# Kernel tuning notes

Hardware: AMD Instinct MI355X
Metric: run time of the kernel (lower is better)

The kernel has to match this reference:

```python
import jax, jax.numpy as jnp
import numpy as np

N_BINS = 15  # matches ECELoss(n_bins=15)


def setup_inputs() -> dict:
    key = jax.random.key(0)
    k1, k2 = jax.random.split(key)
    B, C = 2_097_152, 16
    logits = jax.random.normal(k1, (B, C), dtype=jnp.float32) * 2.0
    # binary multi-label targets, stored as float (forward casts to float anyway)
    targets = (jax.random.uniform(k2, (B, C)) < 0.5).astype(jnp.float32)
    return {"logits": logits, "targets": targets}


def reference(logits, targets):
    """Vectorized ECE: single bucketize + segment-sum pass replacing the
    per-class/per-bin Python loops. Same math: for each non-empty (class, bin)
    cell, accumulate |mean_conf - mean_acc| * (cell_count / B), then divide by
    the number of non-empty cells."""
    B, C = logits.shape
    probs = jax.nn.sigmoid(logits)  # [B, C]
    boundaries = jnp.linspace(0.0, 1.0, N_BINS + 1)
    # bin b satisfies boundaries[b] <= p < boundaries[b+1]  (>= start, < end)
    bin_idx = jnp.searchsorted(boundaries, probs, side="right") - 1  # [B, C]
    valid = (bin_idx >= 0) & (bin_idx < N_BINS)  # p == 1.0 falls in no bin
    seg = jnp.where(valid, jnp.arange(C)[None, :] * N_BINS + bin_idx, C * N_BINS)
    seg = seg.reshape(-1)
    num_seg = C * N_BINS + 1  # last segment = dumping ground for invalid
    ones = jnp.ones((B * C,), dtype=probs.dtype)
    cnt = jax.ops.segment_sum(ones, seg, num_segments=num_seg)[:-1]           # [C*n_bins]
    sum_p = jax.ops.segment_sum(probs.reshape(-1), seg, num_segments=num_seg)[:-1]
    sum_t = jax.ops.segment_sum(targets.reshape(-1), seg, num_segments=num_seg)[:-1]
    nonempty = cnt > 0
    safe = jnp.where(nonempty, cnt, 1.0)
    # |avg_confidence - accuracy| * mask.mean()  per non-empty cell
    term = jnp.abs(sum_p / safe - sum_t / safe) * (cnt / B)
    total = jnp.sum(jnp.where(nonempty, term, 0.0))
    count = jnp.sum(nonempty)
    return jnp.where(count > 0, total / count, jnp.zeros((), probs.dtype))
```

## Files before the change

kernel.cpp:

```cpp
#include <hip/hip_runtime.h>
#include <math.h>

#define NC 16
#define NBINS 15
#define NCELL (NC * NBINS)
#define GRID 2048
#define VITERS 16
#define BROWS 2097152.0
#define MAXREP 8

__device__ __forceinline__ void proc1(float x, float tv, int j, int col,
                                      unsigned int* h) {
    const float LOG2E = 1.4426950408889634f;
    float e = __builtin_amdgcn_exp2f(-x * LOG2E);
    float p = __builtin_amdgcn_rcpf(1.0f + e);
    int b = ((int)(p * 15.0f)) & 15;
    unsigned int u =
        (unsigned int)(fmaf(tv, 262144.0f, fmaf(p, 1024.0f, 0.5f)));
    atomicAdd(&h[(b * 4 + j) * 256 + col], u + (1u << 25));
}

__device__ __forceinline__ void proc4(float4 v, float4 t, int col,
                                      unsigned int* h) {
    proc1(v.x, t.x, 0, col, h);
    proc1(v.y, t.y, 1, col, h);
    proc1(v.z, t.z, 2, col, h);
    proc1(v.w, t.w, 3, col, h);
}

__global__ void __launch_bounds__(256, 2) ece_partial(const float4* __restrict__ logits,
                                                      const float4* __restrict__ targets,
                                                      float* __restrict__ ws, int nrep) {
    __shared__ unsigned int h[64 * 256];
#pragma unroll
    for (int r = 0; r < 64; ++r) h[r * 256 + threadIdx.x] = 0u;
    __syncthreads();

    const int tid = blockIdx.x * 256 + threadIdx.x;
    const int S   = GRID * 256;
    const int col = threadIdx.x;

    for (int k = 0; k < VITERS; k += 4) {
        int i0 = tid + k * S;
        int i1 = i0 + S, i2 = i1 + S, i3 = i2 + S;
        float4 a0 = logits[i0], a1 = logits[i1], a2 = logits[i2], a3 = logits[i3];
        float4 b0 = targets[i0], b1 = targets[i1], b2 = targets[i2], b3 = targets[i3];
        proc4(a0, b0, col, h);
        proc4(a1, b1, col, h);
        proc4(a2, b2, col, h);
        proc4(a3, b3, col, h);
    }
    __syncthreads();

    const int idx = threadIdx.x;
    const int b = idx >> 4, c = idx & 15;
    if (b < NBINS) {
        const int q = c >> 2, j = c & 3;
        const unsigned int* const row = &h[(b * 4 + j) * 256 + q];
        unsigned int cnt = 0, tsum = 0, psum = 0;
#pragma unroll
        for (int m = 0; m < 64; ++m) {
            unsigned int v = row[4 * m];
            cnt  += v >> 25;
            tsum += (v >> 18) & 127u;
            psum += v & 0x3FFFFu;
        }
        float* r = ws + (blockIdx.x & (nrep - 1)) * (3 * NCELL);
        atomicAdd(&r[idx],             (float)cnt);
        atomicAdd(&r[NCELL + idx],     (float)psum * (1.0f / 1024.0f));
        atomicAdd(&r[2 * NCELL + idx], (float)tsum);
    }
}

__global__ void __launch_bounds__(256) ece_final(const float* __restrict__ ws,
                                                 float* __restrict__ out, int nrep) {
    __shared__ double s_term[256];
    __shared__ int s_ne[256];
    int i = threadIdx.x;
    double term = 0.0;
    int ne = 0;
    if (i < NCELL) {
        float cnt = 0.0f, sp = 0.0f, st = 0.0f;
        for (int rep = 0; rep < nrep; ++rep) {
            const float* r = ws + rep * (3 * NCELL);
            cnt += r[i];
            sp  += r[NCELL + i];
            st  += r[2 * NCELL + i];
        }
        if (cnt > 0.0f) {
            ne = 1;
            term = fabs((double)sp / (double)cnt - (double)st / (double)cnt) *
                   ((double)cnt / BROWS);
        }
    }
    s_term[i] = term;
    s_ne[i] = ne;
    __syncthreads();
    for (int off = 128; off > 0; off >>= 1) {
        if (i < off) {
            s_term[i] += s_term[i + off];
            s_ne[i]   += s_ne[i + off];
        }
        __syncthreads();
    }
    if (i == 0) out[0] = (s_ne[0] > 0) ? (float)(s_term[0] / (double)s_ne[0]) : 0.0f;
}

extern "C" void kernel_launch(void* const* d_in, const int* in_sizes, int n_in,
                              void* d_out, int out_size, void* d_ws, size_t ws_size,
                              hipStream_t stream) {
    const float4* logits  = (const float4*)d_in[0];
    const float4* targets = (const float4*)d_in[1];
    float* ws  = (float*)d_ws;
    float* out = (float*)d_out;

    int nrep = MAXREP;
    while (nrep > 1 && (size_t)(nrep * 3 * NCELL * sizeof(float)) > ws_size) nrep >>= 1;

    (void)hipMemsetAsync(ws, 0, nrep * 3 * NCELL * sizeof(float), stream);
    ece_partial<<<GRID, 256, 0, stream>>>(logits, targets, ws, nrep);
    ece_final<<<1, 256, 0, stream>>>(ws, out, nrep);
}
```

Measured before the change: 284.9 us.

## Replace LDS atomic histogram with register bins reduced by DPP row sums

Drops the per-thread LDS histogram and its atomics. Each lane now builds masked one-hot values for all 15 bins per column, sums them across each 16-lane DPP row, and accumulates into registers. The grid grows to 8192 blocks doing 4 iterations each, and the number of global replica slots rises to 64 to spread the float atomics. This removes LDS atomic contention and the large shared-memory footprint, but adds 15×4 DPP reductions per element group, which costs much more ALU work, and raises register pressure.

```diff
diff --git a/kernel.cpp b/kernel.cpp
--- a/kernel.cpp
+++ b/kernel.cpp
@@ -4,71 +4,96 @@
 #define NC 16
 #define NBINS 15
 #define NCELL (NC * NBINS)
-#define GRID 2048
-#define VITERS 16
+#define GRID 8192
+#define K 4
 #define BROWS 2097152.0
-#define MAXREP 8
+#define MAXREP 64
 
-__device__ __forceinline__ void proc1(float x, float tv, int j, int col,
-                                      unsigned int* h) {
-    const float LOG2E = 1.4426950408889634f;
-    float e = __builtin_amdgcn_exp2f(-x * LOG2E);
-    float p = __builtin_amdgcn_rcpf(1.0f + e);
-    int b = ((int)(p * 15.0f)) & 15;
-    unsigned int u =
-        (unsigned int)(fmaf(tv, 262144.0f, fmaf(p, 1024.0f, 0.5f)));
-    atomicAdd(&h[(b * 4 + j) * 256 + col], u + (1u << 25));
+template <int CTRL>
+__device__ __forceinline__ unsigned int dpp_add(unsigned int v) {
+    return v + (unsigned int)__builtin_amdgcn_update_dpp(0, (int)v, CTRL, 0xF, 0xF, true);
 }
 
-__device__ __forceinline__ void proc4(float4 v, float4 t, int col,
-                                      unsigned int* h) {
-    proc1(v.x, t.x, 0, col, h);
-    proc1(v.y, t.y, 1, col, h);
-    proc1(v.z, t.z, 2, col, h);
-    proc1(v.w, t.w, 3, col, h);
-}
+__global__ void __launch_bounds__(256, 2)
+ece_partial(const float4* __restrict__ logits,
+            const float4* __restrict__ targets,
+            float* __restrict__ ws, int nrep) {
+    const int lane = threadIdx.x & 63;
+    const int widx = threadIdx.x >> 6;
+    const int gw   = blockIdx.x * 4 + widx;
+    const int off  = (lane >> 4) + 4 * (lane & 15);
 
-__global__ void __launch_bounds__(256, 2) ece_partial(const float4* __restrict__ logits,
-                                                      const float4* __restrict__ targets,
-                                                      float* __restrict__ ws, int nrep) {
-    __shared__ unsigned int h[64 * 256];
+    float4 la[K], ta[K];
 #pragma unroll
-    for (int r = 0; r < 64; ++r) h[r * 256 + threadIdx.x] = 0u;
-    __syncthreads();
+    for (int k = 0; k < K; ++k) {
+        int idx = (k * (GRID * 4) + gw) * 64 + off;
+        la[k] = logits[idx];
+        ta[k] = targets[idx];
+    }
 
-    const int tid = blockIdx.x * 256 + threadIdx.x;
-    const int S   = GRID * 256;
-    const int col = threadIdx.x;
+    unsigned int acc[4][NBINS];
+#pragma unroll
+    for (int j = 0; j < 4; ++j)
+#pragma unroll
+        for (int b = 0; b < NBINS; ++b) acc[j][b] = 0u;
 
-    for (int k = 0; k < VITERS; k += 4) {
-        int i0 = tid + k * S;
-        int i1 = i0 + S, i2 = i1 + S, i3 = i2 + S;
-        float4 a0 = logits[i0], a1 = logits[i1], a2 = logits[i2], a3 = logits[i3];
-        float4 b0 = targets[i0], b1 = targets[i1], b2 = targets[i2], b3 = targets[i3];
-        proc4(a0, b0, col, h);
-        proc4(a1, b1, col, h);
-        proc4(a2, b2, col, h);
-        proc4(a3, b3, col, h);
+    const float LOG2E = 1.4426950408889634f;
+#pragma unroll
+    for (int k = 0; k < K; ++k) {
+        float xs[4]  = {la[k].x, la[k].y, la[k].z, la[k].w};
+        float tvs[4] = {ta[k].x, ta[k].y, ta[k].z, ta[k].w};
+        int bs[4];
+        unsigned int us[4];
+#pragma unroll
+        for (int j = 0; j < 4; ++j) {
+            float e = __builtin_amdgcn_exp2f(-xs[j] * LOG2E);
+            float p = __builtin_amdgcn_rcpf(1.0f + e);
+            bs[j] = (int)(p * 15.0f);
+            us[j] = (unsigned int)(fmaf(tvs[j], 262144.0f,
+                                        fmaf(p, 1024.0f, 0.5f))) + (1u << 25);
+        }
+#pragma unroll
+        for (int j = 0; j < 4; ++j) {
+#pragma unroll
+            for (int b = 0; b < NBINS; ++b) {
+                unsigned int v = (bs[j] == b) ? us[j] : 0u;
+                v = dpp_add<0x111>(v);
+                v = dpp_add<0x112>(v);
+                v = dpp_add<0x114>(v);
+                v = dpp_add<0x118>(v);
+                acc[j][b] += v;
+            }
+        }
+    }
+
+    __shared__ unsigned int fl[4][4 * NBINS][4];
+    if ((lane & 15) == 15) {
+        const int r = lane >> 4;
+#pragma unroll
+        for (int j = 0; j < 4; ++j)
+#pragma unroll
+            for (int b = 0; b < NBINS; ++b)
+                fl[widx][j * NBINS + b][r] = acc[j][b];
     }
     __syncthreads();
 
-    const int idx = threadIdx.x;
-    const int b = idx >> 4, c = idx & 15;
-    if (b < NBINS) {
-        const int q = c >> 2, j = c & 3;
-        const unsigned int* const row = &h[(b * 4 + j) * 256 + q];
+    const int t = threadIdx.x;
+    if (t < NCELL) {
+        const int bb = t >> 4;
+        const int c  = t & 15;
+        const int r  = c >> 2, j = c & 3;
         unsigned int cnt = 0, tsum = 0, psum = 0;
 #pragma unroll
-        for (int m = 0; m < 64; ++m) {
-            unsigned int v = row[4 * m];
+        for (int w = 0; w < 4; ++w) {
+            unsigned int v = fl[w][j * NBINS + bb][r];
             cnt  += v >> 25;
             tsum += (v >> 18) & 127u;
             psum += v & 0x3FFFFu;
         }
-        float* r = ws + (blockIdx.x & (nrep - 1)) * (3 * NCELL);
-        atomicAdd(&r[idx],             (float)cnt);
-        atomicAdd(&r[NCELL + idx],     (float)psum * (1.0f / 1024.0f));
-        atomicAdd(&r[2 * NCELL + idx], (float)tsum);
+        float* rp = ws + (blockIdx.x & (nrep - 1)) * (3 * NCELL);
+        atomicAdd(&rp[t],             (float)cnt);
+        atomicAdd(&rp[NCELL + t],     (float)psum * (1.0f / 1024.0f));
+        atomicAdd(&rp[2 * NCELL + t], (float)tsum);
     }
 }
 
```

Result: slower. 1.071 ms (+275.9%).
